# Kernel tuning notes

Measured on AMD Instinct MI355X. Metric: run time of the kernel, lower is better.

The kernel has to match this reference:

```python
import jax, jax.numpy as jnp
import numpy as np

N_E, N_U, N_D = 512, 256, 256
N_A = 16
N_FB = 4
N_SV = 256
N_PV = 64
D_IN0 = 3 * (4 * N_A) + 2 * 4   # 200, fb_block output at layer 0
D_IN = 3 * N_SV + 2 * N_PV      # 896, fb_block output thereafter


def _fb_block(s_v, p_v):
    # s_v: (n_e, d_s); p_v: (n_e, n_e, d_p)
    n_e = N_U + N_D
    su_m = jnp.tile(s_v[:N_U].mean(0)[None, :], (n_e, 1))
    sd_m = jnp.tile(s_v[N_U:].mean(0)[None, :], (n_e, 1))
    pu_m = p_v[:N_U].mean(0)   # (n_e, d_p)
    pd_m = p_v[N_U:].mean(0)
    return jnp.concatenate([su_m, sd_m, pu_m, pd_m, s_v], axis=-1)


def setup_inputs() -> dict:
    key = jax.random.key(0)
    ks = jax.random.split(key, 16)

    def lin(k, fin, fout):
        k1, k2 = jax.random.split(k)
        lim = 1.0 / np.sqrt(fin)
        W = jax.random.uniform(k1, (fin, fout), minval=-lim, maxval=lim, dtype=jnp.float32)
        b = jax.random.uniform(k2, (fout,), minval=-lim, maxval=lim, dtype=jnp.float32)
        return W, b

    V0_W, V0_b = lin(ks[0], D_IN0, N_SV)
    W0_W, W0_b = lin(ks[1], 4, N_PV)
    VrW, Vrb, WrW, Wrb = [], [], [], []
    for i in range(N_FB - 1):
        w, b = lin(ks[2 + i], D_IN, N_SV); VrW.append(w); Vrb.append(b)
        w, b = lin(ks[6 + i], N_PV, N_PV); WrW.append(w); Wrb.append(b)
    Vr_W, Vr_b = jnp.stack(VrW), jnp.stack(Vrb)
    Wr_W, Wr_b = jnp.stack(WrW), jnp.stack(Wrb)
    Vhu_W, Vhu_b = lin(ks[10], D_IN, N_SV)
    Vhd_W, Vhd_b = lin(ks[11], D_IN, N_SV)
    wu_W, wu_b = lin(ks[12], N_SV, N_U)
    wd_W, wd_b = lin(ks[13], N_SV, N_D)
    r = jax.random.normal(ks[14], (N_E, 3), dtype=jnp.float32)
    a = jax.random.normal(ks[15], (N_A, 3), dtype=jnp.float32) * 2.0
    return dict(r=r, a=a, V0_W=V0_W, V0_b=V0_b, Vr_W=Vr_W, Vr_b=Vr_b,
                W0_W=W0_W, W0_b=W0_b, Wr_W=Wr_W, Wr_b=Wr_b,
                Vhu_W=Vhu_W, Vhu_b=Vhu_b, Vhd_W=Vhd_W, Vhd_b=Vhd_b,
                wu_W=wu_W, wu_b=wu_b, wd_W=wd_W, wd_b=wd_b)


def reference(r, a, V0_W, V0_b, Vr_W, Vr_b, W0_W, W0_b, Wr_W, Wr_b,
              Vhu_W, Vhu_b, Vhd_W, Vhd_b, wu_W, wu_b, wd_W, wd_b):
    n_e = N_E
    eye = jnp.eye(n_e, dtype=r.dtype)[:, :, None]
    ra = r[:, None, :] - a[None, :, :]                       # (n_e, n_a, 3)
    ra_len = jnp.linalg.norm(ra, axis=-1, keepdims=True)
    rr = r[None, :, :] - r[:, None, :]                       # (n_e, n_e, 3)
    rr_len = jnp.linalg.norm(rr + eye, axis=-1, keepdims=True)
    s_v = jnp.concatenate([ra, ra_len], axis=-1).reshape(n_e, -1)   # (n_e, 4*n_a)
    p_v = jnp.concatenate([rr, rr_len], axis=-1)                    # (n_e, n_e, 4)
    s_blk = _fb_block(s_v, p_v)
    for l in range(N_FB):
        VW, Vb = (V0_W, V0_b) if l == 0 else (Vr_W[l - 1], Vr_b[l - 1])
        WW, Wb = (W0_W, W0_b) if l == 0 else (Wr_W[l - 1], Wr_b[l - 1])
        s_new = jnp.tanh(s_blk @ VW + Vb)
        s_v = s_new + s_v if s_v.shape[-1] == N_SV else s_new   # residual skips layer 0
        p_new = jnp.tanh(p_v @ WW + Wb)
        p_v = p_new + p_v if p_v.shape[-1] == N_PV else p_new
        s_blk = _fb_block(s_v, p_v)
    s_u = jnp.tanh(s_blk[:N_U] @ Vhu_W + Vhu_b)
    s_d = jnp.tanh(s_blk[N_U:] @ Vhd_W + Vhd_b)
    s_wu = s_u @ wu_W + wu_b                                  # (n_u, n_u)
    s_wd = s_d @ wd_W + wd_b                                  # (n_d, n_d)
    exp_u = jnp.linalg.norm(ra[:N_U], axis=-1, keepdims=True)  # (n_u, n_a, 1)
    exp_d = jnp.linalg.norm(ra[N_U:], axis=-1, keepdims=True)
    orb_u = (s_wu * jnp.exp(-exp_u).sum(axis=1))[None]         # (1, n_u, n_u)
    orb_d = (s_wd * jnp.exp(-exp_d).sum(axis=1))[None]
    # logabssumdet with n_det == 1, matrix dim > 1
    sgn_u, log_u = jnp.linalg.slogdet(orb_u)
    sgn_d, log_d = jnp.linalg.slogdet(orb_d)
    psi = (sgn_u * sgn_d * jnp.exp(log_u + log_d)).sum()
    return jnp.log(jnp.abs(psi))
```

## Files before the change

kernel.cpp:

```cpp
#include <hip/hip_runtime.h>
#include <hip/hip_bf16.h>

#define NE 512

__device__ __align__(16) float g_p[2][NE*NE*64];
__device__ __align__(16) float g_sv0[NE*64];
__device__ __align__(16) float g_sv[2][NE*256];
__device__ __align__(16) float g_pu4[NE*4];
__device__ __align__(16) float g_pd4[NE*4];
__device__ __align__(16) float g_pu[NE*64];
__device__ __align__(16) float g_pd[NE*64];
__device__ __align__(16) float g_su0[64];
__device__ __align__(16) float g_sd0[64];
__device__ __align__(16) float g_su[256];
__device__ __align__(16) float g_sd[256];
__device__ __align__(16) float g_part[8*NE*64];
__device__ __align__(16) float g_f[NE];
__device__ __align__(16) float g_hu[256*256];
__device__ __align__(16) float g_hd[256*256];
__device__ __align__(16) float g_orbu[256*256];
__device__ __align__(16) float g_orbd[256*256];
__device__ float g_logs[2];

__device__ __forceinline__ float tanh_fast(float x) {
  float e = __expf(2.f * x);
  return 1.f - 2.f / (e + 1.f);
}

__global__ __launch_bounds__(256) void k_pgeom(const float* __restrict__ r,
                                               const float* __restrict__ a) {
  int j = blockIdx.x, t = threadIdx.x;
  if (j == 0) {
    for (int h = 0; h < 2; ++h) {
      int e = h*256 + t;
      float rx = r[3*e], ry = r[3*e+1], rz = r[3*e+2];
      float facc = 0.f;
      #pragma unroll
      for (int at = 0; at < 16; ++at) {
        float dx = rx - a[3*at], dy = ry - a[3*at+1], dz = rz - a[3*at+2];
        float len = sqrtf(dx*dx + dy*dy + dz*dz);
        g_sv0[e*64 + 4*at + 0] = dx;
        g_sv0[e*64 + 4*at + 1] = dy;
        g_sv0[e*64 + 4*at + 2] = dz;
        g_sv0[e*64 + 4*at + 3] = len;
        facc += expf(-len);
      }
      g_f[e] = facc;
    }
    __syncthreads();
    if (t < 128) {
      int h = t >> 6, c = t & 63;
      float s = 0.f;
      for (int i = 0; i < 256; ++i) s += g_sv0[(h*256 + i)*64 + c];
      (h ? g_sd0 : g_su0)[c] = s * (1.f/256.f);
    }
    __syncthreads();
  }
  float rjx = r[3*j], rjy = r[3*j+1], rjz = r[3*j+2];
  __shared__ float red[4][4];
  for (int h = 0; h < 2; ++h) {
    int i = h*256 + t;
    float dx = rjx - r[3*i], dy = rjy - r[3*i+1], dz = rjz - r[3*i+2];
    float ee = (i == j) ? 1.f : 0.f;
    float ex = dx+ee, ey = dy+ee, ez = dz+ee;
    float len = sqrtf(ex*ex + ey*ey + ez*ez);
    float v0 = dx, v1 = dy, v2 = dz, v3 = len;
    #pragma unroll
    for (int m = 1; m < 64; m <<= 1) {
      v0 += __shfl_xor(v0, m); v1 += __shfl_xor(v1, m);
      v2 += __shfl_xor(v2, m); v3 += __shfl_xor(v3, m);
    }
    if ((t & 63) == 0) {
      int wv = t >> 6;
      red[wv][0]=v0; red[wv][1]=v1; red[wv][2]=v2; red[wv][3]=v3;
    }
    __syncthreads();
    if (t == 0) {
      float* dst = h ? g_pd4 : g_pu4;
      #pragma unroll
      for (int c = 0; c < 4; ++c)
        dst[j*4 + c] = (red[0][c]+red[1][c]+red[2][c]+red[3][c]) * (1.f/256.f);
    }
    __syncthreads();
  }
}

template<int MODE>
__global__ __launch_bounds__(256) void k_pup(const float* __restrict__ W,
                                             const float* __restrict__ Wb,
                                             const float* __restrict__ r,
                                             int src, int dst) {
  __shared__ __align__(16) float psh[4][64];
  int t = threadIdx.x, lane = t & 63, wv = t >> 6;
  int gw = blockIdx.x*4 + wv;
  int j = gw >> 3, chunk = gw & 7;
  int i0 = chunk * 64;
  float macc = 0.f;
  if (MODE == 0) {
    float w0 = W[lane], w1 = W[64+lane], w2 = W[128+lane], w3 = W[192+lane];
    float bb = Wb[lane];
    float rjx = r[3*j], rjy = r[3*j+1], rjz = r[3*j+2];
    float* pout = g_p[0];
    for (int ii = 0; ii < 64; ++ii) {
      int i = i0 + ii;
      float dx = rjx - r[3*i], dy = rjy - r[3*i+1], dz = rjz - r[3*i+2];
      float ee = (i == j) ? 1.f : 0.f;
      float ex = dx+ee, ey = dy+ee, ez = dz+ee;
      float len = sqrtf(ex*ex + ey*ey + ez*ez);
      float y = tanh_fast(bb + dx*w0 + dy*w1 + dz*w2 + len*w3);
      pout[(i*NE + j)*64 + lane] = y;
      macc += y;
    }
  } else {
    const float* pin = g_p[src];
    float* pout = g_p[dst];
    float wcol[64];
    #pragma unroll
    for (int k = 0; k < 64; ++k) wcol[k] = W[k*64 + lane];
    float bb = Wb[lane];
    for (int ii = 0; ii < 64; ++ii) {
      int i = i0 + ii;
      int base = (i*NE + j)*64;
      float x = pin[base + lane];
      psh[wv][lane] = x;
      float acc = bb;
      #pragma unroll
      for (int g = 0; g < 16; ++g) {
        float4 pv = *(const float4*)&psh[wv][4*g];
        acc += pv.x*wcol[4*g] + pv.y*wcol[4*g+1] + pv.z*wcol[4*g+2] + pv.w*wcol[4*g+3];
      }
      float y = tanh_fast(acc) + x;
      if (MODE == 1) pout[base + lane] = y;
      macc += y;
    }
  }
  g_part[chunk*(NE*64) + j*64 + lane] = macc;
}

__global__ __launch_bounds__(256) void k_reduce(int svsel) {
  int bid = blockIdx.x, t = threadIdx.x;
  if (bid < 256) {
    int idx = bid*256 + t;
    int half = idx >> 15, rem = idx & 32767;
    int j = rem >> 6, l = rem & 63;
    const float* pp = g_part + half*(4*NE*64);
    float s = pp[0*(NE*64)+j*64+l] + pp[1*(NE*64)+j*64+l]
            + pp[2*(NE*64)+j*64+l] + pp[3*(NE*64)+j*64+l];
    (half ? g_pd : g_pu)[j*64 + l] = s * (1.f/256.f);
  } else {
    int h = bid - 256;
    const float* sv = g_sv[svsel];
    float s = 0.f;
    for (int i = 0; i < 256; ++i) s += sv[(h*256 + i)*256 + t];
    (h ? g_sd : g_su)[t] = s * (1.f/256.f);
  }
}

template<int PUK, int SVK, int MEANK>
__global__ __launch_bounds__(256) void k_smm(int which, const float* __restrict__ W,
                                             const float* __restrict__ Wb,
                                             const float* __restrict__ W2,
                                             const float* __restrict__ Wb2) {
  constexpr int MAINK = 2*PUK + SVK;
  __shared__ __align__(16) float wsl[MAINK*32];
  __shared__ float insl[32*(MAINK+1)];
  __shared__ float biasv[32];
  __shared__ float bred[256];
  const float *pu_p=nullptr, *pd_p=nullptr, *sv_p=nullptr, *su_p=nullptr, *sd_p=nullptr;
  const float *res_p=nullptr, *rs_p=nullptr;
  float* out_p = nullptr;
  int t = threadIdx.x;
  int rg = blockIdx.x, cg = blockIdx.y;
  int grp = 0, rgl = rg;
  if (which >= 4) { grp = rg >> 3; rgl = rg & 7; }
  const float* Wsel = (which >= 4 && grp) ? W2 : W;
  const float* Wbsel = (which >= 4 && grp) ? Wb2 : Wb;
  int in_base = 0, dotanh = 1;
  switch (which) {
    case 0: pu_p=g_pu4; pd_p=g_pd4; su_p=g_su0; sd_p=g_sd0; sv_p=g_sv0;
            out_p=g_sv[0]; in_base=rg*32; break;
    case 1: case 2: case 3:
      pu_p=g_pu; pd_p=g_pd; su_p=g_su; sd_p=g_sd;
      sv_p=g_sv[(which+1)&1]; res_p=sv_p; out_p=g_sv[which&1]; in_base=rg*32; break;
    case 4: pu_p=g_pu; pd_p=g_pd; su_p=g_su; sd_p=g_sd; sv_p=g_sv[1];
            out_p = grp ? g_hd : g_hu; in_base = grp*256 + rgl*32; break;
    default: sv_p = grp ? g_hd : g_hu; out_p = grp ? g_orbd : g_orbu;
             rs_p = g_f + grp*256; in_base = rgl*32; dotanh = 0; break;
  }
  int out_base = (which >= 4) ? rgl*32 : rg*32;
  int col0 = cg * 32;
  for (int idx = t; idx < MAINK*32; idx += 256) {
    int c = idx >> 5, cl = idx & 31;
    wsl[idx] = Wsel[(2*MEANK + c)*256 + col0 + cl];
  }
  for (int rr = 0; rr < 32; ++rr) {
    int row = in_base + rr;
    for (int c = t; c < MAINK; c += 256) {
      float v;
      if (c < PUK) v = pu_p[row*PUK + c];
      else if (c < 2*PUK) v = pd_p[row*PUK + (c - PUK)];
      else v = sv_p[row*SVK + (c - 2*PUK)];
      insl[rr*(MAINK+1) + c] = v;
    }
  }
  {
    int pcol = t & 31, ps = t >> 5;
    float bacc = 0.f;
    if (MEANK > 0) {
      for (int c = ps; c < MEANK; c += 8)
        bacc += su_p[c]*Wsel[c*256 + col0 + pcol] + sd_p[c]*Wsel[(MEANK + c)*256 + col0 + pcol];
    }
    bred[ps*32 + pcol] = bacc;
  }
  __syncthreads();
  if (t < 32) {
    float s = Wbsel[col0 + t];
    #pragma unroll
    for (int p8 = 0; p8 < 8; ++p8) s += bred[p8*32 + t];
    biasv[t] = s;
  }
  __syncthreads();
  int c4 = t & 7, rl = t >> 3;
  float a0 = biasv[4*c4], a1 = biasv[4*c4+1], a2 = biasv[4*c4+2], a3 = biasv[4*c4+3];
  const float* inrow = &insl[rl*(MAINK+1)];
  #pragma unroll 4
  for (int c = 0; c < MAINK; ++c) {
    float iv = inrow[c];
    float4 wv = *(const float4*)&wsl[c*32 + 4*c4];
    a0 += iv*wv.x; a1 += iv*wv.y; a2 += iv*wv.z; a3 += iv*wv.w;
  }
  int rowA = out_base + rl;
  int col = col0 + 4*c4;
  if (dotanh) { a0=tanh_fast(a0); a1=tanh_fast(a1); a2=tanh_fast(a2); a3=tanh_fast(a3); }
  if (res_p) {
    float4 rv = *(const float4*)&res_p[rowA*256 + col];
    a0 += rv.x; a1 += rv.y; a2 += rv.z; a3 += rv.w;
  }
  if (rs_p) { float fsc = rs_p[rowA]; a0*=fsc; a1*=fsc; a2*=fsc; a3*=fsc; }
  float4 ov; ov.x=a0; ov.y=a1; ov.z=a2; ov.w=a3;
  *(float4*)&out_p[rowA*256 + col] = ov;
}

#define REP8(M) M(0) M(1) M(2) M(3) M(4) M(5) M(6) M(7)
#define DPPMAX(v, CTRL) { unsigned _o = (unsigned)__builtin_amdgcn_update_dpp(0, (int)(v), CTRL, 0xf, 0xf, true); \
                          (v) = (v) > _o ? (v) : _o; }

__global__ __launch_bounds__(1024, 4) void k_lu() {
  __shared__ __align__(16) float colbuf[256];
  __shared__ __align__(16) float prowbuf[32*12];
  const float* A = (blockIdx.x == 0) ? g_orbu : g_orbd;
  int t = threadIdx.x;
  int tile_r = t >> 5;
  int tile_c = t & 31;
  int lane = t & 63;
  int br = tile_r * 8;
  int pb = tile_c * 12;
  const float4* Ap = (const float4*)(A + br*256 + tile_c*8);
#define DECLROW(R) float4 M##R##_0 = Ap[R*64+0], M##R##_1 = Ap[R*64+1];
  REP8(DECLROW)
#undef DECLROW
  unsigned um = 0;
  if (tile_c == 0) {
#define INIT0(R) colbuf[br+R] = M##R##_0.x;
    REP8(INIT0)
#undef INIT0
  }
  __syncthreads();
  float prod = 1.f;
  int esum = 0;
  for (int k = 0; k < 256; ++k) {
    float4 cv = *(const float4*)&colbuf[4*lane];
    float4 ca = *(const float4*)&colbuf[br];
    float4 cb = *(const float4*)&colbuf[br+4];
    unsigned b0 = (um & 1u) ? 0u : ((__float_as_uint(fabsf(cv.x)) & 0xFFFFFF00u) | (unsigned)(4*lane+0));
    unsigned b1 = (um & 2u) ? 0u : ((__float_as_uint(fabsf(cv.y)) & 0xFFFFFF00u) | (unsigned)(4*lane+1));
    unsigned b2 = (um & 4u) ? 0u : ((__float_as_uint(fabsf(cv.z)) & 0xFFFFFF00u) | (unsigned)(4*lane+2));
    unsigned b3 = (um & 8u) ? 0u : ((__float_as_uint(fabsf(cv.w)) & 0xFFFFFF00u) | (unsigned)(4*lane+3));
    unsigned bb = max(max(b0,b1), max(b2,b3));
    DPPMAX(bb, 0x111) DPPMAX(bb, 0x112) DPPMAX(bb, 0x114) DPPMAX(bb, 0x118)
    DPPMAX(bb, 0x142) DPPMAX(bb, 0x143)
    bb = (unsigned)__builtin_amdgcn_readlane((int)bb, 63);
    int p = (int)(bb & 255u);
    int wl = p >> 2, cc = p & 3;
    unsigned px = (unsigned)__builtin_amdgcn_readlane((int)__float_as_uint(cv.x), wl);
    unsigned py = (unsigned)__builtin_amdgcn_readlane((int)__float_as_uint(cv.y), wl);
    unsigned pz = (unsigned)__builtin_amdgcn_readlane((int)__float_as_uint(cv.z), wl);
    unsigned pw = (unsigned)__builtin_amdgcn_readlane((int)__float_as_uint(cv.w), wl);
    float piv = __uint_as_float(cc==0 ? px : cc==1 ? py : cc==2 ? pz : pw);
    int ee; float mant = frexpf(fabsf(piv), &ee);
    prod *= mant; esum += ee;
    int e2; prod = frexpf(prod, &e2); esum += e2;
    if (wl == lane) um |= 1u << cc;
    if (k == 255) break;
    float rp = 1.0f / piv;
    float m0 = ca.x*rp, m1 = ca.y*rp, m2 = ca.z*rp, m3 = ca.w*rp;
    float m4 = cb.x*rp, m5 = cb.y*rp, m6 = cb.z*rp, m7 = cb.w*rp;
    bool alive = (tile_c*8 + 7) > k;
    if (alive && tile_r == (p >> 3)) {
      switch (p & 7) {
#define PUBC(R) case R: *(float4*)&prowbuf[pb+0] = M##R##_0; *(float4*)&prowbuf[pb+4] = M##R##_1; break;
        REP8(PUBC)
#undef PUBC
      }
    }
    __syncthreads();
    if (alive) {
      float4 P0 = *(const float4*)&prowbuf[pb+0];
      float4 P1 = *(const float4*)&prowbuf[pb+4];
#define UPD(R) { float mr = m##R; \
  M##R##_0.x -= mr*P0.x; M##R##_0.y -= mr*P0.y; M##R##_0.z -= mr*P0.z; M##R##_0.w -= mr*P0.w; \
  M##R##_1.x -= mr*P1.x; M##R##_1.y -= mr*P1.y; M##R##_1.z -= mr*P1.z; M##R##_1.w -= mr*P1.w; }
      REP8(UPD)
#undef UPD
      int kn = k + 1;
      if (tile_c == (kn >> 3)) {
        switch (kn & 7) {
#define EXTC(I, G, C) case I: { colbuf[br+0]=M0_##G.C; colbuf[br+1]=M1_##G.C; \
  colbuf[br+2]=M2_##G.C; colbuf[br+3]=M3_##G.C; colbuf[br+4]=M4_##G.C; \
  colbuf[br+5]=M5_##G.C; colbuf[br+6]=M6_##G.C; colbuf[br+7]=M7_##G.C; } break;
          EXTC(0,0,x) EXTC(1,0,y) EXTC(2,0,z) EXTC(3,0,w)
          EXTC(4,1,x) EXTC(5,1,y) EXTC(6,1,z) EXTC(7,1,w)
#undef EXTC
        }
      }
    }
    __syncthreads();
  }
  if (t == 0) g_logs[blockIdx.x] = logf(prod) + (float)esum * 0.69314718055994531f;
}

__global__ void k_final(float* out) { out[0] = g_logs[0] + g_logs[1]; }

extern "C" void kernel_launch(void* const* d_in, const int* in_sizes, int n_in,
                              void* d_out, int out_size, void* d_ws, size_t ws_size,
                              hipStream_t stream) {
  const float* r     = (const float*)d_in[0];
  const float* a     = (const float*)d_in[1];
  const float* V0_W  = (const float*)d_in[2];
  const float* V0_b  = (const float*)d_in[3];
  const float* Vr_W  = (const float*)d_in[4];
  const float* Vr_b  = (const float*)d_in[5];
  const float* W0_W  = (const float*)d_in[6];
  const float* W0_b  = (const float*)d_in[7];
  const float* Wr_W  = (const float*)d_in[8];
  const float* Wr_b  = (const float*)d_in[9];
  const float* Vhu_W = (const float*)d_in[10];
  const float* Vhu_b = (const float*)d_in[11];
  const float* Vhd_W = (const float*)d_in[12];
  const float* Vhd_b = (const float*)d_in[13];
  const float* wu_W  = (const float*)d_in[14];
  const float* wu_b  = (const float*)d_in[15];
  const float* wd_W  = (const float*)d_in[16];
  const float* wd_b  = (const float*)d_in[17];
  float* out = (float*)d_out;

  k_pgeom<<<512, 256, 0, stream>>>(r, a);

  k_smm<4,64,64><<<dim3(16,8), 256, 0, stream>>>(0, V0_W, V0_b, nullptr, nullptr);
  k_pup<0><<<1024, 256, 0, stream>>>(W0_W, W0_b, r, 0, 0);
  k_reduce<<<258, 256, 0, stream>>>(0);
  k_smm<64,256,256><<<dim3(16,8), 256, 0, stream>>>(1, Vr_W + 0*896*256, Vr_b + 0, nullptr, nullptr);
  k_pup<1><<<1024, 256, 0, stream>>>(Wr_W + 0*4096, Wr_b + 0, r, 0, 1);
  k_reduce<<<258, 256, 0, stream>>>(1);
  k_smm<64,256,256><<<dim3(16,8), 256, 0, stream>>>(2, Vr_W + 1*896*256, Vr_b + 256, nullptr, nullptr);
  k_pup<1><<<1024, 256, 0, stream>>>(Wr_W + 1*4096, Wr_b + 64, r, 1, 0);
  k_reduce<<<258, 256, 0, stream>>>(0);
  k_smm<64,256,256><<<dim3(16,8), 256, 0, stream>>>(3, Vr_W + 2*896*256, Vr_b + 512, nullptr, nullptr);
  k_pup<2><<<1024, 256, 0, stream>>>(Wr_W + 2*4096, Wr_b + 128, r, 0, 0);
  k_reduce<<<258, 256, 0, stream>>>(1);
  k_smm<64,256,256><<<dim3(16,8), 256, 0, stream>>>(4, Vhu_W, Vhu_b, Vhd_W, Vhd_b);
  k_smm<0,256,0><<<dim3(16,8), 256, 0, stream>>>(6, wu_W, wu_b, wd_W, wd_b);
  k_lu<<<2, 1024, 0, stream>>>();
  k_final<<<1, 1, 0, stream>>>(out);
}
```

Before: 754.7 us.

## Merge per-layer s and p kernels and restructure LU with double-buffered lookahead

Each layer's s-matrix kernel and p-update kernel are merged into one launch, with extra blocks handling the small s GEMM (now K-tiled through shared memory). This lets the two independent stages run concurrently and removes launches. The LU kernel moves to 512 threads with 8x16 register tiles. It uses double-buffered pivot-row and column buffers and computes the next column early, so each step needs one barrier instead of two. The costs are higher register pressure in the LU and more complex pivot bookkeeping.

```diff
diff --git a/kernel.cpp b/kernel.cpp
--- a/kernel.cpp
+++ b/kernel.cpp
@@ -85,56 +85,131 @@
   }
 }
 
-template<int MODE>
-__global__ __launch_bounds__(256) void k_pup(const float* __restrict__ W,
-                                             const float* __restrict__ Wb,
-                                             const float* __restrict__ r,
-                                             int src, int dst) {
+template<int WHICH, int MODE, int PUK, int SVK, int MEANK>
+__global__ __launch_bounds__(256) void k_layer(const float* __restrict__ VW,
+                                               const float* __restrict__ Vb,
+                                               const float* __restrict__ PW,
+                                               const float* __restrict__ Pb,
+                                               const float* __restrict__ r,
+                                               int src, int dst) {
+  constexpr int MAINK = 2*PUK + SVK;
+  __shared__ __align__(16) float wsl[64*32];
+  __shared__ __align__(16) float insl[32*68];
+  __shared__ float biasv[32];
+  __shared__ float bred[256];
   __shared__ __align__(16) float psh[4][64];
-  int t = threadIdx.x, lane = t & 63, wv = t >> 6;
-  int gw = blockIdx.x*4 + wv;
-  int j = gw >> 3, chunk = gw & 7;
-  int i0 = chunk * 64;
-  float macc = 0.f;
-  if (MODE == 0) {
-    float w0 = W[lane], w1 = W[64+lane], w2 = W[128+lane], w3 = W[192+lane];
-    float bb = Wb[lane];
-    float rjx = r[3*j], rjy = r[3*j+1], rjz = r[3*j+2];
-    float* pout = g_p[0];
-    for (int ii = 0; ii < 64; ++ii) {
-      int i = i0 + ii;
-      float dx = rjx - r[3*i], dy = rjy - r[3*i+1], dz = rjz - r[3*i+2];
-      float ee = (i == j) ? 1.f : 0.f;
-      float ex = dx+ee, ey = dy+ee, ez = dz+ee;
-      float len = sqrtf(ex*ex + ey*ey + ez*ez);
-      float y = tanh_fast(bb + dx*w0 + dy*w1 + dz*w2 + len*w3);
-      pout[(i*NE + j)*64 + lane] = y;
-      macc += y;
-    }
+  int bid = blockIdx.x, t = threadIdx.x;
+  if (bid < 128) {
+    int rg = bid >> 3, cg = bid & 7, col0 = cg*32;
+    const float *pu_p, *pd_p, *sv_p, *su_p, *sd_p, *res_p;
+    float* out_p;
+    if constexpr (WHICH == 0) {
+      pu_p=g_pu4; pd_p=g_pd4; su_p=g_su0; sd_p=g_sd0; sv_p=g_sv0; res_p=nullptr; out_p=g_sv[0];
+    } else {
+      pu_p=g_pu; pd_p=g_pd; su_p=g_su; sd_p=g_sd;
+      sv_p=g_sv[(WHICH+1)&1]; res_p=sv_p; out_p=g_sv[WHICH&1];
+    }
+    {
+      int pcol = t & 31, ps = t >> 5;
+      float bacc = 0.f;
+      for (int c = ps; c < MEANK; c += 8)
+        bacc += su_p[c]*VW[c*256 + col0 + pcol] + sd_p[c]*VW[(MEANK + c)*256 + col0 + pcol];
+      bred[ps*32 + pcol] = bacc;
+    }
+    __syncthreads();
+    if (t < 32) {
+      float s = Vb[col0 + t];
+      #pragma unroll
+      for (int p8 = 0; p8 < 8; ++p8) s += bred[p8*32 + t];
+      biasv[t] = s;
+    }
+    __syncthreads();
+    int c4 = t & 7, rl = t >> 3;
+    float a0 = biasv[4*c4], a1 = biasv[4*c4+1], a2 = biasv[4*c4+2], a3 = biasv[4*c4+3];
+    int row_in = rg*32;
+    #pragma unroll
+    for (int c0 = 0; c0 < MAINK; c0 += 64) {
+      const int CL = (MAINK - c0) < 64 ? (MAINK - c0) : 64;
+      for (int idx = t; idx < CL*32; idx += 256) {
+        int c = idx >> 5, cl = idx & 31;
+        wsl[idx] = VW[(2*MEANK + c0 + c)*256 + col0 + cl];
+      }
+      {
+        int rr = t >> 3;
+        for (int c2 = (t & 7); c2 < CL; c2 += 8) {
+          int c = c0 + c2, row = row_in + rr;
+          float v;
+          if (c < PUK) v = pu_p[row*PUK + c];
+          else if (c < 2*PUK) v = pd_p[row*PUK + (c - PUK)];
+          else v = sv_p[row*SVK + (c - 2*PUK)];
+          insl[rr*68 + c2] = v;
+        }
+      }
+      __syncthreads();
+      const float* inrow = &insl[rl*68];
+      #pragma unroll 4
+      for (int c2 = 0; c2 < CL; ++c2) {
+        float iv = inrow[c2];
+        float4 wv = *(const float4*)&wsl[c2*32 + 4*c4];
+        a0 += iv*wv.x; a1 += iv*wv.y; a2 += iv*wv.z; a3 += iv*wv.w;
+      }
+      __syncthreads();
+    }
+    int rowA = rg*32 + rl;
+    int col = col0 + 4*c4;
+    a0 = tanh_fast(a0); a1 = tanh_fast(a1); a2 = tanh_fast(a2); a3 = tanh_fast(a3);
+    if (res_p) {
+      float4 rv = *(const float4*)&res_p[rowA*256 + col];
+      a0 += rv.x; a1 += rv.y; a2 += rv.z; a3 += rv.w;
+    }
+    float4 ov; ov.x=a0; ov.y=a1; ov.z=a2; ov.w=a3;
+    *(float4*)&out_p[rowA*256 + col] = ov;
   } else {
-    const float* pin = g_p[src];
-    float* pout = g_p[dst];
-    float wcol[64];
-    #pragma unroll
-    for (int k = 0; k < 64; ++k) wcol[k] = W[k*64 + lane];
-    float bb = Wb[lane];
-    for (int ii = 0; ii < 64; ++ii) {
-      int i = i0 + ii;
-      int base = (i*NE + j)*64;
-      float x = pin[base + lane];
-      psh[wv][lane] = x;
-      float acc = bb;
+    int lane = t & 63, wv = t >> 6;
+    int gw = (bid - 128)*4 + wv;
+    int j = gw >> 3, chunk = gw & 7;
+    int i0 = chunk * 64;
+    float macc = 0.f;
+    if (MODE == 0) {
+      float w0 = PW[lane], w1 = PW[64+lane], w2 = PW[128+lane], w3 = PW[192+lane];
+      float bb = Pb[lane];
+      float rjx = r[3*j], rjy = r[3*j+1], rjz = r[3*j+2];
+      float* pout = g_p[0];
+      for (int ii = 0; ii < 64; ++ii) {
+        int i = i0 + ii;
+        float dx = rjx - r[3*i], dy = rjy - r[3*i+1], dz = rjz - r[3*i+2];
+        float ee = (i == j) ? 1.f : 0.f;
+        float ex = dx+ee, ey = dy+ee, ez = dz+ee;
+        float len = sqrtf(ex*ex + ey*ey + ez*ez);
+        float y = tanh_fast(bb + dx*w0 + dy*w1 + dz*w2 + len*w3);
+        pout[(i*NE + j)*64 + lane] = y;
+        macc += y;
+      }
+    } else {
+      const float* pin = g_p[src];
+      float* pout = g_p[dst];
+      float wcol[64];
       #pragma unroll
-      for (int g = 0; g < 16; ++g) {
-        float4 pv = *(const float4*)&psh[wv][4*g];
-        acc += pv.x*wcol[4*g] + pv.y*wcol[4*g+1] + pv.z*wcol[4*g+2] + pv.w*wcol[4*g+3];
-      }
-      float y = tanh_fast(acc) + x;
-      if (MODE == 1) pout[base + lane] = y;
-      macc += y;
-    }
-  }
-  g_part[chunk*(NE*64) + j*64 + lane] = macc;
+      for (int k = 0; k < 64; ++k) wcol[k] = PW[k*64 + lane];
+      float bb = Pb[lane];
+      for (int ii = 0; ii < 64; ++ii) {
+        int i = i0 + ii;
+        int base = (i*NE + j)*64;
+        float x = pin[base + lane];
+        psh[wv][lane] = x;
+        float acc = bb;
+        #pragma unroll
+        for (int g = 0; g < 16; ++g) {
+          float4 pv = *(const float4*)&psh[wv][4*g];
+          acc += pv.x*wcol[4*g] + pv.y*wcol[4*g+1] + pv.z*wcol[4*g+2] + pv.w*wcol[4*g+3];
+        }
+        float y = tanh_fast(acc) + x;
+        if (MODE == 1) pout[base + lane] = y;
+        macc += y;
+      }
+    }
+    g_part[chunk*(NE*64) + j*64 + lane] = macc;
+  }
 }
 
 __global__ __launch_bounds__(256) void k_reduce(int svsel) {
@@ -167,27 +242,22 @@
   __shared__ float biasv[32];
   __shared__ float bred[256];
   const float *pu_p=nullptr, *pd_p=nullptr, *sv_p=nullptr, *su_p=nullptr, *sd_p=nullptr;
-  const float *res_p=nullptr, *rs_p=nullptr;
+  const float *rs_p=nullptr;
   float* out_p = nullptr;
   int t = threadIdx.x;
   int rg = blockIdx.x, cg = blockIdx.y;
-  int grp = 0, rgl = rg;
-  if (which >= 4) { grp = rg >> 3; rgl = rg & 7; }
-  const float* Wsel = (which >= 4 && grp) ? W2 : W;
-  const float* Wbsel = (which >= 4 && grp) ? Wb2 : Wb;
+  int grp = rg >> 3, rgl = rg & 7;
+  const float* Wsel = grp ? W2 : W;
+  const float* Wbsel = grp ? Wb2 : Wb;
   int in_base = 0, dotanh = 1;
-  switch (which) {
-    case 0: pu_p=g_pu4; pd_p=g_pd4; su_p=g_su0; sd_p=g_sd0; sv_p=g_sv0;
-            out_p=g_sv[0]; in_base=rg*32; break;
-    case 1: case 2: case 3:
-      pu_p=g_pu; pd_p=g_pd; su_p=g_su; sd_p=g_sd;
-      sv_p=g_sv[(which+1)&1]; res_p=sv_p; out_p=g_sv[which&1]; in_base=rg*32; break;
-    case 4: pu_p=g_pu; pd_p=g_pd; su_p=g_su; sd_p=g_sd; sv_p=g_sv[1];
-            out_p = grp ? g_hd : g_hu; in_base = grp*256 + rgl*32; break;
-    default: sv_p = grp ? g_hd : g_hu; out_p = grp ? g_orbd : g_orbu;
-             rs_p = g_f + grp*256; in_base = rgl*32; dotanh = 0; break;
-  }
-  int out_base = (which >= 4) ? rgl*32 : rg*32;
+  if (which == 4) {
+    pu_p=g_pu; pd_p=g_pd; su_p=g_su; sd_p=g_sd; sv_p=g_sv[1];
+    out_p = grp ? g_hd : g_hu; in_base = grp*256 + rgl*32;
+  } else {
+    sv_p = grp ? g_hd : g_hu; out_p = grp ? g_orbd : g_orbu;
+    rs_p = g_f + grp*256; in_base = rgl*32; dotanh = 0;
+  }
+  int out_base = rgl*32;
   int col0 = cg * 32;
   for (int idx = t; idx < MAINK*32; idx += 256) {
     int c = idx >> 5, cl = idx & 31;
@@ -232,10 +302,6 @@
   int rowA = out_base + rl;
   int col = col0 + 4*c4;
   if (dotanh) { a0=tanh_fast(a0); a1=tanh_fast(a1); a2=tanh_fast(a2); a3=tanh_fast(a3); }
-  if (res_p) {
-    float4 rv = *(const float4*)&res_p[rowA*256 + col];
-    a0 += rv.x; a1 += rv.y; a2 += rv.z; a3 += rv.w;
-  }
   if (rs_p) { float fsc = rs_p[rowA]; a0*=fsc; a1*=fsc; a2*=fsc; a3*=fsc; }
   float4 ov; ov.x=a0; ov.y=a1; ov.z=a2; ov.w=a3;
   *(float4*)&out_p[rowA*256 + col] = ov;
@@ -245,33 +311,51 @@
 #define DPPMAX(v, CTRL) { unsigned _o = (unsigned)__builtin_amdgcn_update_dpp(0, (int)(v), CTRL, 0xf, 0xf, true); \
                           (v) = (v) > _o ? (v) : _o; }
 
-__global__ __launch_bounds__(1024, 4) void k_lu() {
-  __shared__ __align__(16) float colbuf[256];
-  __shared__ __align__(16) float prowbuf[32*12];
+__global__ __launch_bounds__(512, 2) void k_lu() {
+  __shared__ __align__(16) float colbuf[2][256];
+  __shared__ __align__(16) float prowbuf[2][16*20];
   const float* A = (blockIdx.x == 0) ? g_orbu : g_orbd;
   int t = threadIdx.x;
-  int tile_r = t >> 5;
-  int tile_c = t & 31;
+  int tile_c = t >> 5;
+  int tile_r = t & 31;
   int lane = t & 63;
   int br = tile_r * 8;
-  int pb = tile_c * 12;
-  const float4* Ap = (const float4*)(A + br*256 + tile_c*8);
-#define DECLROW(R) float4 M##R##_0 = Ap[R*64+0], M##R##_1 = Ap[R*64+1];
+  int pb = tile_c * 20;
+  const float4* Ap = (const float4*)(A + br*256 + tile_c*16);
+#define DECLROW(R) float4 M##R##_0 = Ap[R*64+0], M##R##_1 = Ap[R*64+1], \
+                          M##R##_2 = Ap[R*64+2], M##R##_3 = Ap[R*64+3];
   REP8(DECLROW)
 #undef DECLROW
   unsigned um = 0;
   if (tile_c == 0) {
-#define INIT0(R) colbuf[br+R] = M##R##_0.x;
+#define INIT0(R) colbuf[0][br+R] = M##R##_0.x;
     REP8(INIT0)
 #undef INIT0
   }
   __syncthreads();
   float prod = 1.f;
   int esum = 0;
+  float m0=0,m1=0,m2=0,m3=0,m4=0,m5=0,m6=0,m7=0;
   for (int k = 0; k < 256; ++k) {
-    float4 cv = *(const float4*)&colbuf[4*lane];
-    float4 ca = *(const float4*)&colbuf[br];
-    float4 cb = *(const float4*)&colbuf[br+4];
+    const float* cbin = colbuf[k & 1];
+    float4 cv = *(const float4*)&cbin[4*lane];
+    float4 ca = *(const float4*)&cbin[br];
+    float4 cb2 = *(const float4*)&cbin[br+4];
+    bool aliveU = (tile_c*16 + 15) >= k;
+    if (k > 0 && aliveU) {
+      const float* pwp = &prowbuf[(k-1) & 1][pb];
+      float4 P0 = *(const float4*)&pwp[0];
+      float4 P1 = *(const float4*)&pwp[4];
+      float4 P2 = *(const float4*)&pwp[8];
+      float4 P3 = *(const float4*)&pwp[12];
+#define UPD(R) { float mr = m##R; \
+  M##R##_0.x -= mr*P0.x; M##R##_0.y -= mr*P0.y; M##R##_0.z -= mr*P0.z; M##R##_0.w -= mr*P0.w; \
+  M##R##_1.x -= mr*P1.x; M##R##_1.y -= mr*P1.y; M##R##_1.z -= mr*P1.z; M##R##_1.w -= mr*P1.w; \
+  M##R##_2.x -= mr*P2.x; M##R##_2.y -= mr*P2.y; M##R##_2.z -= mr*P2.z; M##R##_2.w -= mr*P2.w; \
+  M##R##_3.x -= mr*P3.x; M##R##_3.y -= mr*P3.y; M##R##_3.z -= mr*P3.z; M##R##_3.w -= mr*P3.w; }
+      REP8(UPD)
+#undef UPD
+    }
     unsigned b0 = (um & 1u) ? 0u : ((__float_as_uint(fabsf(cv.x)) & 0xFFFFFF00u) | (unsigned)(4*lane+0));
     unsigned b1 = (um & 2u) ? 0u : ((__float_as_uint(fabsf(cv.y)) & 0xFFFFFF00u) | (unsigned)(4*lane+1));
     unsigned b2 = (um & 4u) ? 0u : ((__float_as_uint(fabsf(cv.z)) & 0xFFFFFF00u) | (unsigned)(4*lane+2));
@@ -293,36 +377,43 @@
     if (wl == lane) um |= 1u << cc;
     if (k == 255) break;
     float rp = 1.0f / piv;
-    float m0 = ca.x*rp, m1 = ca.y*rp, m2 = ca.z*rp, m3 = ca.w*rp;
-    float m4 = cb.x*rp, m5 = cb.y*rp, m6 = cb.z*rp, m7 = cb.w*rp;
-    bool alive = (tile_c*8 + 7) > k;
-    if (alive && tile_r == (p >> 3)) {
+    m0 = ca.x*rp; m1 = ca.y*rp; m2 = ca.z*rp; m3 = ca.w*rp;
+    m4 = cb2.x*rp; m5 = cb2.y*rp; m6 = cb2.z*rp; m7 = cb2.w*rp;
+    bool aliveK = (tile_c*16 + 15) > k;
+    if (aliveK && tile_r == (p >> 3)) {
+      float* pw_ = &prowbuf[k & 1][pb];
       switch (p & 7) {
-#define PUBC(R) case R: *(float4*)&prowbuf[pb+0] = M##R##_0; *(float4*)&prowbuf[pb+4] = M##R##_1; break;
+#define PUBC(R) case R: *(float4*)&pw_[0] = M##R##_0; *(float4*)&pw_[4] = M##R##_1; \
+                        *(float4*)&pw_[8] = M##R##_2; *(float4*)&pw_[12] = M##R##_3; break;
         REP8(PUBC)
 #undef PUBC
       }
     }
-    __syncthreads();
-    if (alive) {
-      float4 P0 = *(const float4*)&prowbuf[pb+0];
-      float4 P1 = *(const float4*)&prowbuf[pb+4];
-#define UPD(R) { float mr = m##R; \
-  M##R##_0.x -= mr*P0.x; M##R##_0.y -= mr*P0.y; M##R##_0.z -= mr*P0.z; M##R##_0.w -= mr*P0.w; \
-  M##R##_1.x -= mr*P1.x; M##R##_1.y -= mr*P1.y; M##R##_1.z -= mr*P1.z; M##R##_1.w -= mr*P1.w; }
-      REP8(UPD)
-#undef UPD
-      int kn = k + 1;
-      if (tile_c == (kn >> 3)) {
-        switch (kn & 7) {
-#define EXTC(I, G, C) case I: { colbuf[br+0]=M0_##G.C; colbuf[br+1]=M1_##G.C; \
-  colbuf[br+2]=M2_##G.C; colbuf[br+3]=M3_##G.C; colbuf[br+4]=M4_##G.C; \
-  colbuf[br+5]=M5_##G.C; colbuf[br+6]=M6_##G.C; colbuf[br+7]=M7_##G.C; } break;
-          EXTC(0,0,x) EXTC(1,0,y) EXTC(2,0,z) EXTC(3,0,w)
-          EXTC(4,1,x) EXTC(5,1,y) EXTC(6,1,z) EXTC(7,1,w)
+    int kn = k + 1;
+    if (tile_c == (kn >> 4)) {
+      float e0,e1,e2b,e3,e4,e5,e6,e7;
+      switch (kn & 15) {
+#define EXTC(I, G, C) case I: e0=M0_##G.C; e1=M1_##G.C; e2b=M2_##G.C; e3=M3_##G.C; \
+                              e4=M4_##G.C; e5=M5_##G.C; e6=M6_##G.C; e7=M7_##G.C; break;
+        EXTC(0,0,x) EXTC(1,0,y) EXTC(2,0,z) EXTC(3,0,w)
+        EXTC(4,1,x) EXTC(5,1,y) EXTC(6,1,z) EXTC(7,1,w)
+        EXTC(8,2,x) EXTC(9,2,y) EXTC(10,2,z) EXTC(11,2,w)
+        EXTC(12,3,x) EXTC(13,3,y) EXTC(14,3,z) EXTC(15,3,w)
 #undef EXTC
-        }
-      }
+      }
+      float sel;
+      switch (p & 7) {
+        case 0: sel = e0; break; case 1: sel = e1; break;
+        case 2: sel = e2b; break; case 3: sel = e3; break;
+        case 4: sel = e4; break; case 5: sel = e5; break;
+        case 6: sel = e6; break; default: sel = e7; break;
+      }
+      float pv = __shfl(sel, (tile_c & 1)*32 + (p >> 3), 64);
+      float4 w0, w1;
+      w0.x = e0 - m0*pv; w0.y = e1 - m1*pv; w0.z = e2b - m2*pv; w0.w = e3 - m3*pv;
+      w1.x = e4 - m4*pv; w1.y = e5 - m5*pv; w1.z = e6 - m6*pv; w1.w = e7 - m7*pv;
+      *(float4*)&colbuf[kn & 1][br] = w0;
+      *(float4*)&colbuf[kn & 1][br+4] = w1;
     }
     __syncthreads();
   }
@@ -356,20 +447,19 @@
 
   k_pgeom<<<512, 256, 0, stream>>>(r, a);
 
-  k_smm<4,64,64><<<dim3(16,8), 256, 0, stream>>>(0, V0_W, V0_b, nullptr, nullptr);
-  k_pup<0><<<1024, 256, 0, stream>>>(W0_W, W0_b, r, 0, 0);
+  k_layer<0,0,4,64,64><<<1152, 256, 0, stream>>>(V0_W, V0_b, W0_W, W0_b, r, 0, 0);
   k_reduce<<<258, 256, 0, stream>>>(0);
-  k_smm<64,256,256><<<dim3(16,8), 256, 0, stream>>>(1, Vr_W + 0*896*256, Vr_b + 0, nullptr, nullptr);
-  k_pup<1><<<1024, 256, 0, stream>>>(Wr_W + 0*4096, Wr_b + 0, r, 0, 1);
+  k_layer<1,1,64,256,256><<<1152, 256, 0, stream>>>(Vr_W + 0*896*256, Vr_b + 0,
+                                                    Wr_W + 0*4096, Wr_b + 0, r, 0, 1);
   k_reduce<<<258, 256, 0, stream>>>(1);
-  k_smm<64,256,256><<<dim3(16,8), 256, 0, stream>>>(2, Vr_W + 1*896*256, Vr_b + 256, nullptr, nullptr);
-  k_pup<1><<<1024, 256, 0, stream>>>(Wr_W + 1*4096, Wr_b + 64, r, 1, 0);
+  k_layer<2,1,64,256,256><<<1152, 256, 0, stream>>>(Vr_W + 1*896*256, Vr_b + 256,
+                                                    Wr_W + 1*4096, Wr_b + 64, r, 1, 0);
   k_reduce<<<258, 256, 0, stream>>>(0);
-  k_smm<64,256,256><<<dim3(16,8), 256, 0, stream>>>(3, Vr_W + 2*896*256, Vr_b + 512, nullptr, nullptr);
-  k_pup<2><<<1024, 256, 0, stream>>>(Wr_W + 2*4096, Wr_b + 128, r, 0, 0);
+  k_layer<3,2,64,256,256><<<1152, 256, 0, stream>>>(Vr_W + 2*896*256, Vr_b + 512,
+                                                    Wr_W + 2*4096, Wr_b + 128, r, 0, 0);
   k_reduce<<<258, 256, 0, stream>>>(1);
   k_smm<64,256,256><<<dim3(16,8), 256, 0, stream>>>(4, Vhu_W, Vhu_b, Vhd_W, Vhd_b);
   k_smm<0,256,0><<<dim3(16,8), 256, 0, stream>>>(6, wu_W, wu_b, wd_W, wd_b);
-  k_lu<<<2, 1024, 0, stream>>>();
+  k_lu<<<2, 512, 0, stream>>>();
   k_final<<<1, 1, 0, stream>>>(out);
 }
```

After: 636.6 us. -15.6%, faster.

## Fuse pairwise-feature layers into one LDS-resident kernel and restructure LU pipeline

Applied to the files above, without the earlier changes.

All four pairwise-feature layers now run in a single kernel that keeps each wave's 32x64 slice in LDS. This removes the 64 MB per-layer global round-trips of the p tensor. Per-layer partial means are written once and reduced in one kernel, and the s-chain kernels read the mean for their layer index. The LU kernel moves to 512 threads with 8x16 tiles, double-buffered column and pivot-row buffers, deferred trailing updates so only one barrier is needed per step, and less frequent exponent renormalisation. The costs are higher LDS use per block, more registers per thread in the LU, and extra complexity in the pivot-column extraction logic.

```diff
diff --git a/kernel.cpp b/kernel.cpp
--- a/kernel.cpp
+++ b/kernel.cpp
@@ -3,18 +3,17 @@
 
 #define NE 512
 
-__device__ __align__(16) float g_p[2][NE*NE*64];
 __device__ __align__(16) float g_sv0[NE*64];
 __device__ __align__(16) float g_sv[2][NE*256];
 __device__ __align__(16) float g_pu4[NE*4];
 __device__ __align__(16) float g_pd4[NE*4];
-__device__ __align__(16) float g_pu[NE*64];
-__device__ __align__(16) float g_pd[NE*64];
+__device__ __align__(16) float g_puL[4*NE*64];
+__device__ __align__(16) float g_pdL[4*NE*64];
 __device__ __align__(16) float g_su0[64];
 __device__ __align__(16) float g_sd0[64];
 __device__ __align__(16) float g_su[256];
 __device__ __align__(16) float g_sd[256];
-__device__ __align__(16) float g_part[8*NE*64];
+__device__ __align__(16) float g_part4[4*16*NE*64];
 __device__ __align__(16) float g_f[NE];
 __device__ __align__(16) float g_hu[256*256];
 __device__ __align__(16) float g_hd[256*256];
@@ -85,82 +84,92 @@
   }
 }
 
-template<int MODE>
-__global__ __launch_bounds__(256) void k_pup(const float* __restrict__ W,
-                                             const float* __restrict__ Wb,
-                                             const float* __restrict__ r,
-                                             int src, int dst) {
-  __shared__ __align__(16) float psh[4][64];
+__global__ __launch_bounds__(256, 4) void k_pchain(const float* __restrict__ W0,
+                                                   const float* __restrict__ b0,
+                                                   const float* __restrict__ Wr,
+                                                   const float* __restrict__ brs,
+                                                   const float* __restrict__ r) {
+  __shared__ __align__(16) float xbuf[4][32*64];
   int t = threadIdx.x, lane = t & 63, wv = t >> 6;
   int gw = blockIdx.x*4 + wv;
-  int j = gw >> 3, chunk = gw & 7;
-  int i0 = chunk * 64;
-  float macc = 0.f;
-  if (MODE == 0) {
-    float w0 = W[lane], w1 = W[64+lane], w2 = W[128+lane], w3 = W[192+lane];
-    float bb = Wb[lane];
-    float rjx = r[3*j], rjy = r[3*j+1], rjz = r[3*j+2];
-    float* pout = g_p[0];
-    for (int ii = 0; ii < 64; ++ii) {
+  int j = gw >> 4, chunk = gw & 15;
+  int i0 = chunk * 32;
+  float* xb = xbuf[wv];
+  float rjx = r[3*j], rjy = r[3*j+1], rjz = r[3*j+2];
+  float macc0 = 0.f, macc1 = 0.f, macc2 = 0.f, macc3 = 0.f;
+  {
+    float w0 = W0[lane], w1 = W0[64+lane], w2 = W0[128+lane], w3 = W0[192+lane];
+    float bb = b0[lane];
+    for (int ii = 0; ii < 32; ++ii) {
       int i = i0 + ii;
       float dx = rjx - r[3*i], dy = rjy - r[3*i+1], dz = rjz - r[3*i+2];
       float ee = (i == j) ? 1.f : 0.f;
       float ex = dx+ee, ey = dy+ee, ez = dz+ee;
       float len = sqrtf(ex*ex + ey*ey + ez*ez);
       float y = tanh_fast(bb + dx*w0 + dy*w1 + dz*w2 + len*w3);
-      pout[(i*NE + j)*64 + lane] = y;
-      macc += y;
-    }
-  } else {
-    const float* pin = g_p[src];
-    float* pout = g_p[dst];
+      xb[ii*64 + lane] = y;
+      macc0 += y;
+    }
+  }
+  for (int l = 0; l < 3; ++l) {
+    const float* W = Wr + l*4096;
     float wcol[64];
     #pragma unroll
     for (int k = 0; k < 64; ++k) wcol[k] = W[k*64 + lane];
-    float bb = Wb[lane];
-    for (int ii = 0; ii < 64; ++ii) {
-      int i = i0 + ii;
-      int base = (i*NE + j)*64;
-      float x = pin[base + lane];
-      psh[wv][lane] = x;
+    float bb = brs[l*64 + lane];
+    float mac = 0.f;
+    for (int ii = 0; ii < 32; ++ii) {
+      const float* row = &xb[ii*64];
+      float x = row[lane];
       float acc = bb;
       #pragma unroll
       for (int g = 0; g < 16; ++g) {
-        float4 pv = *(const float4*)&psh[wv][4*g];
+        float4 pv = *(const float4*)&row[4*g];
         acc += pv.x*wcol[4*g] + pv.y*wcol[4*g+1] + pv.z*wcol[4*g+2] + pv.w*wcol[4*g+3];
       }
       float y = tanh_fast(acc) + x;
-      if (MODE == 1) pout[base + lane] = y;
-      macc += y;
-    }
-  }
-  g_part[chunk*(NE*64) + j*64 + lane] = macc;
-}
-
-__global__ __launch_bounds__(256) void k_reduce(int svsel) {
-  int bid = blockIdx.x, t = threadIdx.x;
-  if (bid < 256) {
-    int idx = bid*256 + t;
-    int half = idx >> 15, rem = idx & 32767;
-    int j = rem >> 6, l = rem & 63;
-    const float* pp = g_part + half*(4*NE*64);
-    float s = pp[0*(NE*64)+j*64+l] + pp[1*(NE*64)+j*64+l]
-            + pp[2*(NE*64)+j*64+l] + pp[3*(NE*64)+j*64+l];
-    (half ? g_pd : g_pu)[j*64 + l] = s * (1.f/256.f);
-  } else {
-    int h = bid - 256;
-    const float* sv = g_sv[svsel];
-    float s = 0.f;
-    for (int i = 0; i < 256; ++i) s += sv[(h*256 + i)*256 + t];
-    (h ? g_sd : g_su)[t] = s * (1.f/256.f);
-  }
+      xb[ii*64 + lane] = y;
+      mac += y;
+    }
+    if (l == 0) macc1 = mac;
+    else if (l == 1) macc2 = mac;
+    else macc3 = mac;
+  }
+  int base = chunk*(NE*64) + j*64 + lane;
+  g_part4[0*(16*NE*64) + base] = macc0;
+  g_part4[1*(16*NE*64) + base] = macc1;
+  g_part4[2*(16*NE*64) + base] = macc2;
+  g_part4[3*(16*NE*64) + base] = macc3;
+}
+
+__global__ __launch_bounds__(256) void k_reduce_p() {
+  int idx = blockIdx.x*256 + threadIdx.x;
+  int l = idx >> 16;
+  int rem = idx & 65535;
+  int half = rem >> 15;
+  int r2 = rem & 32767;
+  int j = r2 >> 6, c = r2 & 63;
+  const float* pp = g_part4 + l*(16*NE*64) + half*(8*NE*64) + j*64 + c;
+  float s = 0.f;
+  #pragma unroll
+  for (int ch = 0; ch < 8; ++ch) s += pp[ch*(NE*64)];
+  (half ? g_pdL : g_puL)[l*(NE*64) + j*64 + c] = s * (1.f/256.f);
+}
+
+__global__ __launch_bounds__(256) void k_smean(int svsel) {
+  int h = blockIdx.x, t = threadIdx.x;
+  const float* sv = g_sv[svsel];
+  float s = 0.f;
+  for (int i = 0; i < 256; ++i) s += sv[(h*256 + i)*256 + t];
+  (h ? g_sd : g_su)[t] = s * (1.f/256.f);
 }
 
 template<int PUK, int SVK, int MEANK>
 __global__ __launch_bounds__(256) void k_smm(int which, const float* __restrict__ W,
                                              const float* __restrict__ Wb,
                                              const float* __restrict__ W2,
-                                             const float* __restrict__ Wb2) {
+                                             const float* __restrict__ Wb2,
+                                             int pl) {
   constexpr int MAINK = 2*PUK + SVK;
   __shared__ __align__(16) float wsl[MAINK*32];
   __shared__ float insl[32*(MAINK+1)];
@@ -180,10 +189,10 @@
     case 0: pu_p=g_pu4; pd_p=g_pd4; su_p=g_su0; sd_p=g_sd0; sv_p=g_sv0;
             out_p=g_sv[0]; in_base=rg*32; break;
     case 1: case 2: case 3:
-      pu_p=g_pu; pd_p=g_pd; su_p=g_su; sd_p=g_sd;
+      pu_p=g_puL + pl*(NE*64); pd_p=g_pdL + pl*(NE*64); su_p=g_su; sd_p=g_sd;
       sv_p=g_sv[(which+1)&1]; res_p=sv_p; out_p=g_sv[which&1]; in_base=rg*32; break;
-    case 4: pu_p=g_pu; pd_p=g_pd; su_p=g_su; sd_p=g_sd; sv_p=g_sv[1];
-            out_p = grp ? g_hd : g_hu; in_base = grp*256 + rgl*32; break;
+    case 4: pu_p=g_puL + pl*(NE*64); pd_p=g_pdL + pl*(NE*64); su_p=g_su; sd_p=g_sd;
+            sv_p=g_sv[1]; out_p = grp ? g_hd : g_hu; in_base = grp*256 + rgl*32; break;
     default: sv_p = grp ? g_hd : g_hu; out_p = grp ? g_orbd : g_orbu;
              rs_p = g_f + grp*256; in_base = rgl*32; dotanh = 0; break;
   }
@@ -245,33 +254,51 @@
 #define DPPMAX(v, CTRL) { unsigned _o = (unsigned)__builtin_amdgcn_update_dpp(0, (int)(v), CTRL, 0xf, 0xf, true); \
                           (v) = (v) > _o ? (v) : _o; }
 
-__global__ __launch_bounds__(1024, 4) void k_lu() {
-  __shared__ __align__(16) float colbuf[256];
-  __shared__ __align__(16) float prowbuf[32*12];
+__global__ __launch_bounds__(512, 2) void k_lu() {
+  __shared__ __align__(16) float colbuf[2][256];
+  __shared__ __align__(16) float prowbuf[2][16*20];
   const float* A = (blockIdx.x == 0) ? g_orbu : g_orbd;
   int t = threadIdx.x;
-  int tile_r = t >> 5;
-  int tile_c = t & 31;
+  int tile_c = t >> 5;
+  int tile_r = t & 31;
   int lane = t & 63;
   int br = tile_r * 8;
-  int pb = tile_c * 12;
-  const float4* Ap = (const float4*)(A + br*256 + tile_c*8);
-#define DECLROW(R) float4 M##R##_0 = Ap[R*64+0], M##R##_1 = Ap[R*64+1];
+  int pb = tile_c * 20;
+  const float4* Ap = (const float4*)(A + br*256 + tile_c*16);
+#define DECLROW(R) float4 M##R##_0 = Ap[R*64+0], M##R##_1 = Ap[R*64+1], \
+                          M##R##_2 = Ap[R*64+2], M##R##_3 = Ap[R*64+3];
   REP8(DECLROW)
 #undef DECLROW
   unsigned um = 0;
   if (tile_c == 0) {
-#define INIT0(R) colbuf[br+R] = M##R##_0.x;
+#define INIT0(R) colbuf[0][br+R] = M##R##_0.x;
     REP8(INIT0)
 #undef INIT0
   }
   __syncthreads();
   float prod = 1.f;
   int esum = 0;
+  float m0=0,m1=0,m2=0,m3=0,m4=0,m5=0,m6=0,m7=0;
   for (int k = 0; k < 256; ++k) {
-    float4 cv = *(const float4*)&colbuf[4*lane];
-    float4 ca = *(const float4*)&colbuf[br];
-    float4 cb = *(const float4*)&colbuf[br+4];
+    const float* cbin = colbuf[k & 1];
+    float4 cv = *(const float4*)&cbin[4*lane];
+    float4 ca = *(const float4*)&cbin[br];
+    float4 cb2 = *(const float4*)&cbin[br+4];
+    bool aliveU = (tile_c*16 + 15) >= k;
+    if (k > 0 && aliveU) {
+      const float* pwp = &prowbuf[(k-1) & 1][pb];
+      float4 P0 = *(const float4*)&pwp[0];
+      float4 P1 = *(const float4*)&pwp[4];
+      float4 P2 = *(const float4*)&pwp[8];
+      float4 P3 = *(const float4*)&pwp[12];
+#define UPD(R) { float mr = m##R; \
+  M##R##_0.x -= mr*P0.x; M##R##_0.y -= mr*P0.y; M##R##_0.z -= mr*P0.z; M##R##_0.w -= mr*P0.w; \
+  M##R##_1.x -= mr*P1.x; M##R##_1.y -= mr*P1.y; M##R##_1.z -= mr*P1.z; M##R##_1.w -= mr*P1.w; \
+  M##R##_2.x -= mr*P2.x; M##R##_2.y -= mr*P2.y; M##R##_2.z -= mr*P2.z; M##R##_2.w -= mr*P2.w; \
+  M##R##_3.x -= mr*P3.x; M##R##_3.y -= mr*P3.y; M##R##_3.z -= mr*P3.z; M##R##_3.w -= mr*P3.w; }
+      REP8(UPD)
+#undef UPD
+    }
     unsigned b0 = (um & 1u) ? 0u : ((__float_as_uint(fabsf(cv.x)) & 0xFFFFFF00u) | (unsigned)(4*lane+0));
     unsigned b1 = (um & 2u) ? 0u : ((__float_as_uint(fabsf(cv.y)) & 0xFFFFFF00u) | (unsigned)(4*lane+1));
     unsigned b2 = (um & 4u) ? 0u : ((__float_as_uint(fabsf(cv.z)) & 0xFFFFFF00u) | (unsigned)(4*lane+2));
@@ -289,40 +316,49 @@
     float piv = __uint_as_float(cc==0 ? px : cc==1 ? py : cc==2 ? pz : pw);
     int ee; float mant = frexpf(fabsf(piv), &ee);
     prod *= mant; esum += ee;
-    int e2; prod = frexpf(prod, &e2); esum += e2;
+    if ((k & 31) == 31) { int e2; prod = frexpf(prod, &e2); esum += e2; }
     if (wl == lane) um |= 1u << cc;
     if (k == 255) break;
     float rp = 1.0f / piv;
-    float m0 = ca.x*rp, m1 = ca.y*rp, m2 = ca.z*rp, m3 = ca.w*rp;
-    float m4 = cb.x*rp, m5 = cb.y*rp, m6 = cb.z*rp, m7 = cb.w*rp;
-    bool alive = (tile_c*8 + 7) > k;
-    if (alive && tile_r == (p >> 3)) {
+    m0 = ca.x*rp; m1 = ca.y*rp; m2 = ca.z*rp; m3 = ca.w*rp;
+    m4 = cb2.x*rp; m5 = cb2.y*rp; m6 = cb2.z*rp; m7 = cb2.w*rp;
+    bool aliveK = (tile_c*16 + 15) > k;
+    if (aliveK && tile_r == (p >> 3)) {
+      float* pw_ = &prowbuf[k & 1][pb];
       switch (p & 7) {
-#define PUBC(R) case R: *(float4*)&prowbuf[pb+0] = M##R##_0; *(float4*)&prowbuf[pb+4] = M##R##_1; break;
+#define PUBC(R) case R: *(float4*)&pw_[0] = M##R##_0; *(float4*)&pw_[4] = M##R##_1; \
+                        *(float4*)&pw_[8] = M##R##_2; *(float4*)&pw_[12] = M##R##_3; break;
         REP8(PUBC)
 #undef PUBC
       }
     }
-    __syncthreads();
-    if (alive) {
-      float4 P0 = *(const float4*)&prowbuf[pb+0];
-      float4 P1 = *(const float4*)&prowbuf[pb+4];
-#define UPD(R) { float mr = m##R; \
-  M##R##_0.x -= mr*P0.x; M##R##_0.y -= mr*P0.y; M##R##_0.z -= mr*P0.z; M##R##_0.w -= mr*P0.w; \
-  M##R##_1.x -= mr*P1.x; M##R##_1.y -= mr*P1.y; M##R##_1.z -= mr*P1.z; M##R##_1.w -= mr*P1.w; }
-      REP8(UPD)
-#undef UPD
-      int kn = k + 1;
-      if (tile_c == (kn >> 3)) {
-        switch (kn & 7) {
-#define EXTC(I, G, C) case I: { colbuf[br+0]=M0_##G.C; colbuf[br+1]=M1_##G.C; \
-  colbuf[br+2]=M2_##G.C; colbuf[br+3]=M3_##G.C; colbuf[br+4]=M4_##G.C; \
-  colbuf[br+5]=M5_##G.C; colbuf[br+6]=M6_##G.C; colbuf[br+7]=M7_##G.C; } break;
-          EXTC(0,0,x) EXTC(1,0,y) EXTC(2,0,z) EXTC(3,0,w)
-          EXTC(4,1,x) EXTC(5,1,y) EXTC(6,1,z) EXTC(7,1,w)
+    int kn = k + 1;
+    if (tile_c == (kn >> 4)) {
+      float e0,e1,e2b,e3,e4,e5,e6,e7;
+      switch (kn & 15) {
+#define EXTC(I, G, C) case I: e0=M0_##G.C; e1=M1_##G.C; e2b=M2_##G.C; e3=M3_##G.C; \
+                              e4=M4_##G.C; e5=M5_##G.C; e6=M6_##G.C; e7=M7_##G.C; break;
+        EXTC(0,0,x) EXTC(1,0,y) EXTC(2,0,z) EXTC(3,0,w)
+        EXTC(4,1,x) EXTC(5,1,y) EXTC(6,1,z) EXTC(7,1,w)
+        EXTC(8,2,x) EXTC(9,2,y) EXTC(10,2,z) EXTC(11,2,w)
+        EXTC(12,3,x) EXTC(13,3,y) EXTC(14,3,z) EXTC(15,3,w)
 #undef EXTC
-        }
       }
+      float sel;
+      switch (p & 7) {
+        case 0: sel = e0; break; case 1: sel = e1; break;
+        case 2: sel = e2b; break; case 3: sel = e3; break;
+        case 4: sel = e4; break; case 5: sel = e5; break;
+        case 6: sel = e6; break; default: sel = e7; break;
+      }
+      int srcl = __builtin_amdgcn_readfirstlane((tile_c & 1)*32 + (p >> 3));
+      float pv = __uint_as_float((unsigned)__builtin_amdgcn_readlane(
+                   (int)__float_as_uint(sel), srcl));
+      float4 w0, w1;
+      w0.x = e0 - m0*pv; w0.y = e1 - m1*pv; w0.z = e2b - m2*pv; w0.w = e3 - m3*pv;
+      w1.x = e4 - m4*pv; w1.y = e5 - m5*pv; w1.z = e6 - m6*pv; w1.w = e7 - m7*pv;
+      *(float4*)&colbuf[kn & 1][br] = w0;
+      *(float4*)&colbuf[kn & 1][br+4] = w1;
     }
     __syncthreads();
   }
@@ -355,21 +391,22 @@
   float* out = (float*)d_out;
 
   k_pgeom<<<512, 256, 0, stream>>>(r, a);
-
-  k_smm<4,64,64><<<dim3(16,8), 256, 0, stream>>>(0, V0_W, V0_b, nullptr, nullptr);
-  k_pup<0><<<1024, 256, 0, stream>>>(W0_W, W0_b, r, 0, 0);
-  k_reduce<<<258, 256, 0, stream>>>(0);
-  k_smm<64,256,256><<<dim3(16,8), 256, 0, stream>>>(1, Vr_W + 0*896*256, Vr_b + 0, nullptr, nullptr);
-  k_pup<1><<<1024, 256, 0, stream>>>(Wr_W + 0*4096, Wr_b + 0, r, 0, 1);
-  k_reduce<<<258, 256, 0, stream>>>(1);
-  k_smm<64,256,256><<<dim3(16,8), 256, 0, stream>>>(2, Vr_W + 1*896*256, Vr_b + 256, nullptr, nullptr);
-  k_pup<1><<<1024, 256, 0, stream>>>(Wr_W + 1*4096, Wr_b + 64, r, 1, 0);
-  k_reduce<<<258, 256, 0, stream>>>(0);
-  k_smm<64,256,256><<<dim3(16,8), 256, 0, stream>>>(3, Vr_W + 2*896*256, Vr_b + 512, nullptr, nullptr);
-  k_pup<2><<<1024, 256, 0, stream>>>(Wr_W + 2*4096, Wr_b + 128, r, 0, 0);
-  k_reduce<<<258, 256, 0, stream>>>(1);
-  k_smm<64,256,256><<<dim3(16,8), 256, 0, stream>>>(4, Vhu_W, Vhu_b, Vhd_W, Vhd_b);
-  k_smm<0,256,0><<<dim3(16,8), 256, 0, stream>>>(6, wu_W, wu_b, wd_W, wd_b);
-  k_lu<<<2, 1024, 0, stream>>>();
+  k_pchain<<<2048, 256, 0, stream>>>(W0_W, W0_b, Wr_W, Wr_b, r);
+  k_reduce_p<<<1024, 256, 0, stream>>>();
+
+  k_smm<4,64,64><<<dim3(16,8), 256, 0, stream>>>(0, V0_W, V0_b, nullptr, nullptr, 0);
+  k_smean<<<2, 256, 0, stream>>>(0);
+  k_smm<64,256,256><<<dim3(16,8), 256, 0, stream>>>(1, Vr_W + 0*896*256, Vr_b + 0,
+                                                    nullptr, nullptr, 0);
+  k_smean<<<2, 256, 0, stream>>>(1);
+  k_smm<64,256,256><<<dim3(16,8), 256, 0, stream>>>(2, Vr_W + 1*896*256, Vr_b + 256,
+                                                    nullptr, nullptr, 1);
+  k_smean<<<2, 256, 0, stream>>>(0);
+  k_smm<64,256,256><<<dim3(16,8), 256, 0, stream>>>(3, Vr_W + 2*896*256, Vr_b + 512,
+                                                    nullptr, nullptr, 2);
+  k_smean<<<2, 256, 0, stream>>>(1);
+  k_smm<64,256,256><<<dim3(16,8), 256, 0, stream>>>(4, Vhu_W, Vhu_b, Vhd_W, Vhd_b, 3);
+  k_smm<0,256,0><<<dim3(16,8), 256, 0, stream>>>(6, wu_W, wu_b, wd_W, wd_b, 0);
+  k_lu<<<2, 512, 0, stream>>>();
   k_final<<<1, 1, 0, stream>>>(out);
 }
```

Result: faster. 650.9 us (-13.8%).
